# Kernel optimization log

Hardware: AMD Instinct MI355X
Metric: run time of the kernel (lower is better)

## Reference

```python
import jax, jax.numpy as jnp
import numpy as np

B, H, W = 64, 128, 128
K_SIS, K_RANGE = 0.5, 0.3
PSI_SCALE = 0.05
SKIP_W = 0.1
ALPHA_MAX = 0.5
SIGMA, KSIZE = 1.0, 5
DN = ('NCHW', 'OIHW', 'NCHW')


def conv2d(x, w, b, pad):
    y = jax.lax.conv_general_dilated(x, w, (1, 1), [(pad, pad), (pad, pad)], dimension_numbers=DN)
    return y + b[None, :, None, None]


def group_norm(x, groups, gamma, beta, eps=1e-5):
    Bc, C, Hc, Wc = x.shape
    xr = x.reshape(Bc, groups, C // groups, Hc, Wc)
    mu = xr.mean(axis=(2, 3, 4), keepdims=True)
    var = xr.var(axis=(2, 3, 4), keepdims=True)
    xn = ((xr - mu) / jnp.sqrt(var + eps)).reshape(Bc, C, Hc, Wc)
    return xn * gamma[None, :, None, None] + beta[None, :, None, None]


def coords():
    xs = jnp.linspace(-1.0, 1.0, W)
    ys = jnp.linspace(-1.0, 1.0, H)
    X, Y = jnp.meshgrid(xs, ys, indexing='xy')  # (H, W)
    r = jnp.sqrt(X * X + Y * Y)
    phi = jnp.arctan2(Y, X)
    polar = jnp.stack([r, jnp.cos(phi), jnp.sin(phi)], axis=0)  # (3,H,W)
    base_grid = jnp.stack([X, Y], axis=-1)  # (H,W,2)
    return polar, r, base_grid


def gaussian_blur(x):
    off = jnp.arange(KSIZE, dtype=jnp.float32) - (KSIZE - 1) / 2.0
    k1 = jnp.exp(-off * off / (2.0 * SIGMA * SIGMA))
    k1 = k1 / k1.sum()
    p = KSIZE // 2
    xp = jnp.pad(x, ((0, 0), (0, 0), (p, p), (p, p)), mode='reflect')
    xh = jax.lax.conv_general_dilated(xp, k1.reshape(1, 1, 1, KSIZE), (1, 1), [(0, 0), (0, 0)], dimension_numbers=DN)
    return jax.lax.conv_general_dilated(xh, k1.reshape(1, 1, KSIZE, 1), (1, 1), [(0, 0), (0, 0)], dimension_numbers=DN)


def grad_x(a, dx):  # along W (last axis), np.gradient style
    left = a[..., 1:2] - a[..., 0:1]
    mid = (a[..., 2:] - a[..., :-2]) * 0.5
    right = a[..., -1:] - a[..., -2:-1]
    return jnp.concatenate([left, mid, right], axis=-1) / dx


def grad_y(a, dy):  # along H
    top = a[..., 1:2, :] - a[..., 0:1, :]
    mid = (a[..., 2:, :] - a[..., :-2, :]) * 0.5
    bot = a[..., -1:, :] - a[..., -2:-1, :]
    return jnp.concatenate([top, mid, bot], axis=-2) / dy


def soft_clamp(a):
    return ALPHA_MAX * jnp.tanh(a / ALPHA_MAX)


def grid_sample_bilinear_border(img, grid):
    # img (B,1,H,W), grid (B,H,W,2) in [-1,1], align_corners=True, border pad
    Bc, _, Hc, Wc = img.shape
    px = (grid[..., 0] + 1.0) * 0.5 * (Wc - 1)
    py = (grid[..., 1] + 1.0) * 0.5 * (Hc - 1)
    x0 = jnp.floor(px)
    y0 = jnp.floor(py)
    wx = px - x0
    wy = py - y0
    x0i = jnp.clip(x0.astype(jnp.int32), 0, Wc - 1)
    x1i = jnp.clip(x0i + 1, 0, Wc - 1)
    y0i = jnp.clip(y0.astype(jnp.int32), 0, Hc - 1)
    y1i = jnp.clip(y0i + 1, 0, Hc - 1)
    im = img[:, 0]
    bidx = jnp.arange(Bc)[:, None, None]
    g = lambda yy, xx: im[bidx, yy, xx]
    out = (g(y0i, x0i) * (1 - wx) * (1 - wy) + g(y0i, x1i) * wx * (1 - wy)
           + g(y1i, x0i) * (1 - wx) * wy + g(y1i, x1i) * wx * wy)
    return out[:, None, :, :]


def _conv_init(key, shape, scale=None):
    fan_in = shape[1] * shape[2] * shape[3]
    s = scale if scale is not None else 1.0 / np.sqrt(fan_in)
    return jax.random.normal(key, shape, dtype=jnp.float32) * s


def setup_inputs() -> dict:
    key = jax.random.key(0)
    ks = jax.random.split(key, 16)
    d = {'image': jax.random.uniform(ks[0], (B, 1, H, W), dtype=jnp.float32)}
    # KPredictor params
    d['kw1'] = _conv_init(ks[1], (32, 4, 3, 3)); d['kb1'] = jnp.zeros((32,), jnp.float32)
    d['kg1'] = jnp.ones((32,), jnp.float32); d['kbeta1'] = jnp.zeros((32,), jnp.float32)
    d['kw2'] = _conv_init(ks[2], (32, 32, 3, 3)); d['kb2'] = jnp.zeros((32,), jnp.float32)
    d['kg2'] = jnp.ones((32,), jnp.float32); d['kbeta2'] = jnp.zeros((32,), jnp.float32)
    d['kw3'] = _conv_init(ks[3], (16, 32, 3, 3)); d['kb3'] = jnp.zeros((16,), jnp.float32)
    d['kg3'] = jnp.ones((16,), jnp.float32); d['kbeta3'] = jnp.zeros((16,), jnp.float32)
    d['kw4'] = _conv_init(ks[4], (1, 16, 1, 1), scale=0.02); d['kb4'] = jnp.zeros((1,), jnp.float32)
    # PsiResidualPredictor params
    d['pw1'] = _conv_init(ks[5], (16, 4, 3, 3)); d['pb1'] = jnp.zeros((16,), jnp.float32)
    d['pg1'] = jnp.ones((16,), jnp.float32); d['pbeta1'] = jnp.zeros((16,), jnp.float32)
    d['pw2'] = _conv_init(ks[6], (16, 16, 3, 3)); d['pb2'] = jnp.zeros((16,), jnp.float32)
    d['pg2'] = jnp.ones((16,), jnp.float32); d['pbeta2'] = jnp.zeros((16,), jnp.float32)
    d['pw3'] = _conv_init(ks[7], (1, 16, 1, 1), scale=0.02); d['pb3'] = jnp.zeros((1,), jnp.float32)
    return d


def _forward(image, kw1, kb1, kg1, kbeta1, kw2, kb2, kg2, kbeta2, kw3, kb3, kg3, kbeta3,
             kw4, kb4, pw1, pb1, pg1, pbeta1, pw2, pb2, pg2, pbeta2, pw3, pb3):
    polar, theta_abs, base_grid = coords()
    x = jnp.concatenate([image, jnp.broadcast_to(polar[None], (image.shape[0], 3, H, W))], axis=1)
    silu = jax.nn.silu
    # k predictor
    h = silu(group_norm(conv2d(x, kw1, kb1, 1), 8, kg1, kbeta1))
    h = silu(group_norm(conv2d(h, kw2, kb2, 1), 8, kg2, kbeta2))
    h = silu(group_norm(conv2d(h, kw3, kb3, 1), 4, kg3, kbeta3))
    k = K_SIS * (1.0 + K_RANGE * jnp.tanh(conv2d(h, kw4, kb4, 0)))
    # psi residual predictor
    p = silu(group_norm(conv2d(x, pw1, pb1, 1), 4, pg1, pbeta1))
    p = silu(group_norm(conv2d(p, pw2, pb2, 1), 4, pg2, pbeta2))
    psi_res = PSI_SCALE * jnp.tanh(conv2d(p, pw3, pb3, 0))
    psi = k * theta_abs[None, None] + psi_res
    psi_s = gaussian_blur(psi)
    dx = 2.0 / (W - 1)
    dy = 2.0 / (H - 1)
    alpha_x = soft_clamp(grad_x(psi_s, dx))
    alpha_y = soft_clamp(grad_y(psi_s, dy))
    alpha_grid = jnp.stack([alpha_x[:, 0], alpha_y[:, 0]], axis=-1)  # (B,H,W,2)
    beta_grid = jnp.clip(base_grid[None] - alpha_grid, -1.0, 1.0)
    warped = grid_sample_bilinear_border(image, beta_grid)
    source = (1.0 - SKIP_W) * warped + SKIP_W * image
    return source, k, psi, alpha_x, alpha_y


def reference(image, kw1, kb1, kg1, kbeta1, kw2, kb2, kg2, kbeta2, kw3, kb3, kg3, kbeta3,
              kw4, kb4, pw1, pb1, pg1, pbeta1, pw2, pb2, pg2, pbeta2, pw3, pb3):
    return _forward(image, kw1, kb1, kg1, kbeta1, kw2, kb2, kg2, kbeta2, kw3, kb3, kg3,
                    kbeta3, kw4, kb4, pw1, pb1, pg1, pbeta1, pw2, pb2, pg2, pbeta2, pw3, pb3)
```

## Files before the change

kernel.cpp:

```cpp
#include <hip/hip_runtime.h>

static constexpr int H = 128, W = 128, HW = H * W;

typedef __attribute__((ext_vector_type(8))) short short8;
typedef __attribute__((ext_vector_type(4))) float f32x4;
typedef unsigned int uint;
typedef unsigned short ushort;

__device__ __forceinline__ float silu_f(float v) { return v / (1.f + __expf(-v)); }
__device__ __forceinline__ ushort f2bf(float f) {
    uint u = __builtin_bit_cast(uint, f);
    return (ushort)((u + 0x7FFFu + ((u >> 16) & 1u)) >> 16);
}
__device__ __forceinline__ float bf2f(ushort s) {
    return __builtin_bit_cast(float, (uint)s << 16);
}

struct PrepArgs {
    const float *w1, *w2, *w3, *wp1, *wp2;
    float *wt1, *wtp1, *polar, *stats;
    ushort *wpk2h, *wpk2l, *wpk3h, *wpk3l, *wpkph, *wpkpl;
    int nstats;
};

__global__ void prep_k(PrepArgs a) {
    int tid = blockIdx.x * 256 + threadIdx.x;
    int stride = gridDim.x * 256;
    for (int i = tid; i < a.nstats; i += stride) a.stats[i] = 0.f;
    for (int i = tid; i < HW; i += stride) {
        int yy = i >> 7, xx = i & 127;
        float X = -1.f + 2.f * xx / 127.f;
        float Y = -1.f + 2.f * yy / 127.f;
        float r = sqrtf(X * X + Y * Y);
        float inv = (r > 0.f) ? 1.f / r : 0.f;
        a.polar[i] = r;
        a.polar[HW + i] = (r > 0.f) ? X * inv : 1.f;
        a.polar[2 * HW + i] = Y * inv;
    }
    for (int i = tid; i < 4 * 9 * 32; i += stride) {
        int cout = i / 36, rem = i % 36;
        a.wt1[rem * 32 + cout] = a.w1[i];
    }
    for (int i = tid; i < 4 * 9 * 16; i += stride) {
        int cout = i / 36, rem = i % 36;
        a.wtp1[rem * 16 + cout] = a.wp1[i];
    }
    for (int i = tid; i < 9 * 2 * 64 * 8; i += stride) {
        int j = i & 7, l = (i >> 3) & 63, t = i >> 9;
        int q = t >> 1, nt = t & 1;
        int k = (l >> 4) * 8 + j;
        int n = nt * 16 + (l & 15);
        int ky = q / 3, kx = q % 3;
        float w = a.w2[((n * 32 + k) * 3 + ky) * 3 + kx];
        ushort h = f2bf(w);
        a.wpk2h[i] = h;
        a.wpk2l[i] = f2bf(w - bf2f(h));
    }
    for (int i = tid; i < 9 * 64 * 8; i += stride) {
        int j = i & 7, l = (i >> 3) & 63, q = i >> 9;
        int k = (l >> 4) * 8 + j;
        int n = l & 15;
        int ky = q / 3, kx = q % 3;
        float w = a.w3[((n * 32 + k) * 3 + ky) * 3 + kx];
        ushort h = f2bf(w);
        a.wpk3h[i] = h;
        a.wpk3l[i] = f2bf(w - bf2f(h));
    }
    for (int i = tid; i < 9 * 64 * 8; i += stride) {
        int j = i & 7, l = (i >> 3) & 63, q = i >> 9;
        int k = (l >> 4) * 8 + j;
        int cin = k & 15;
        int n = l & 15;
        float w = a.wp2[((n * 16 + cin) * 3 + q / 3) * 3 + q % 3];
        ushort h = f2bf(w);
        a.wpkph[i] = h;
        a.wpkpl[i] = f2bf(w - bf2f(h));
    }
}

template <int COUT, int G>
__global__ __launch_bounds__(256) void conv1_k(
    const float* __restrict__ img, const float* __restrict__ polar,
    const float* __restrict__ wt, const float* __restrict__ bias,
    float* __restrict__ outraw, float* __restrict__ stats) {
    const int tid = threadIdx.x;
    const int y = blockIdx.x * 2 + (tid >> 7);
    const int x = tid & 127;
    const int b = blockIdx.y;

    float acc[COUT];
#pragma unroll
    for (int c = 0; c < COUT; c++) acc[c] = bias[c];

#pragma unroll
    for (int cin = 0; cin < 4; cin++) {
        const float* pl = (cin == 0) ? img + (size_t)b * HW : polar + (size_t)(cin - 1) * HW;
#pragma unroll
        for (int ky = 0; ky < 3; ky++) {
            int yy = y + ky - 1;
            if (yy >= 0 && yy < H) {
                const float* row = pl + yy * W;
                float v1 = row[x];
                float v0 = (x > 0) ? row[x - 1] : 0.f;
                float v2 = (x < 127) ? row[x + 1] : 0.f;
                const float* wr = wt + (cin * 9 + ky * 3) * COUT;
#pragma unroll
                for (int c = 0; c < COUT; c++) {
                    acc[c] = fmaf(wr[c], v0, acc[c]);
                    acc[c] = fmaf(wr[COUT + c], v1, acc[c]);
                    acc[c] = fmaf(wr[2 * COUT + c], v2, acc[c]);
                }
            }
        }
    }

    float4* ob = (float4*)(outraw + ((size_t)b * HW + y * W + x) * COUT);
#pragma unroll
    for (int i = 0; i < COUT / 4; i++)
        ob[i] = make_float4(acc[4 * i], acc[4 * i + 1], acc[4 * i + 2], acc[4 * i + 3]);

    constexpr int CgO = COUT / G;
    __shared__ float sred[4][G][2];
    const int lane = tid & 63, wid = tid >> 6;
#pragma unroll
    for (int g = 0; g < G; g++) {
        float s = 0.f, s2 = 0.f;
#pragma unroll
        for (int c = g * CgO; c < (g + 1) * CgO; c++) { s += acc[c]; s2 += acc[c] * acc[c]; }
#pragma unroll
        for (int off = 32; off > 0; off >>= 1) {
            s += __shfl_down(s, off);
            s2 += __shfl_down(s2, off);
        }
        if (lane == 0) { sred[wid][g][0] = s; sred[wid][g][1] = s2; }
    }
    __syncthreads();
    if (tid < G) {
        float s = 0.f, s2 = 0.f;
#pragma unroll
        for (int w = 0; w < 4; w++) { s += sred[w][tid][0]; s2 += sred[w][tid][1]; }
        atomicAdd(&stats[((size_t)b * G + tid) * 2], s);
        atomicAdd(&stats[((size_t)b * G + tid) * 2 + 1], s2);
    }
}

template <int CIN, int COUT, int Gin, int Gout>
__global__ __launch_bounds__(256, 3) void conv_roll_k(
    const float* __restrict__ raw_in, const float* __restrict__ stats_in,
    const float* __restrict__ gamma, const float* __restrict__ beta,
    const float* __restrict__ bias,
    const short8* __restrict__ wph, const short8* __restrict__ wpl,
    float* __restrict__ outraw, float* __restrict__ stats_out) {

    constexpr int LDSC = 2 * CIN;
    constexpr int SWZM = LDSC / 8 - 1;
    constexpr int NCH8 = CIN / 8;
    constexpr int WN = (COUT == 32) ? 2 : 1;
    constexpr int F = (WN == 2) ? 4 : 2;
    constexpr int ROWS = 8;
    constexpr int ROWB = 128 * LDSC * 2;
    constexpr int CHUNKS = 128 * NCH8 / 256;

    __shared__ __align__(16) ushort ring[3 * 128 * LDSC];
    __shared__ float la[CIN], lc[CIN];

    const int tid = threadIdx.x;
    const int wid = tid >> 6, l = tid & 63;
    const int lm = l & 15, lk = l >> 4;
    const int y0 = blockIdx.x * ROWS;
    const int b = blockIdx.y;
    const int wn = (WN == 2) ? (wid & 1) : 0;
    const int pxb = (WN == 2) ? ((wid >> 1) * 64) : (wid * 32);
    const int ch = wn * 16 + lm;

    if (tid < CIN) {
        constexpr float inv = 1.f / ((CIN / Gin) * (float)HW);
        int g = tid / (CIN / Gin);
        float s = stats_in[((size_t)b * Gin + g) * 2];
        float s2 = stats_in[((size_t)b * Gin + g) * 2 + 1];
        float m = s * inv;
        float rs = rsqrtf(s2 * inv - m * m + 1e-5f);
        float aa = gamma[tid] * rs;
        la[tid] = aa;
        lc[tid] = beta[tid] - m * aa;
    }
    __syncthreads();

    short8 wh[9], wl[9];
#pragma unroll
    for (int q = 0; q < 9; q++) {
        wh[q] = wph[(q * WN + wn) * 64 + l];
        wl[q] = wpl[(q * WN + wn) * 64 + l];
    }
    const float bv = bias[ch];
    const short8 Z8 = {0, 0, 0, 0, 0, 0, 0, 0};
    char* tbw = (char*)ring;

    auto load_row = [&](int ys, float4* g0, float4* g1) {
#pragma unroll
        for (int ck = 0; ck < CHUNKS; ck++) {
            int c = tid + ck * 256;
            int px = c / NCH8, ch8 = c % NCH8;
            const float4* gp = (const float4*)(raw_in + (((size_t)b * HW + ys * W + px) * CIN + ch8 * 8));
            g0[ck] = gp[0];
            g1[ck] = gp[1];
        }
    };
    auto stage_row = [&](int ys, int slot, const float4* g0, const float4* g1) {
#pragma unroll
        for (int ck = 0; ck < CHUNKS; ck++) {
            int c = tid + ck * 256;
            int px = c / NCH8, ch8 = c % NCH8;
            short8 hi8, lo8;
            if (ys >= 0 && ys < H) {
                float vv[8] = {g0[ck].x, g0[ck].y, g0[ck].z, g0[ck].w,
                               g1[ck].x, g1[ck].y, g1[ck].z, g1[ck].w};
#pragma unroll
                for (int e = 0; e < 8; e++) {
                    int cc = ch8 * 8 + e;
                    float f = silu_f(fmaf(vv[e], la[cc], lc[cc]));
                    ushort hb = f2bf(f);
                    hi8[e] = (short)hb;
                    lo8[e] = (short)f2bf(f - bf2f(hb));
                }
            } else {
#pragma unroll
                for (int e = 0; e < 8; e++) { hi8[e] = 0; lo8[e] = 0; }
            }
            int inner = px * LDSC * 2 + ch8 * 16;
            int swz = (px & SWZM) << 4;
            char* sb = tbw + slot * ROWB;
            *(short8*)(sb + (inner ^ swz)) = hi8;
            *(short8*)(sb + ((inner + CIN * 2) ^ swz)) = lo8;
        }
    };

    {
        float4 p0[CHUNKS], p1[CHUNKS];
        for (int pr = 0; pr < 3; pr++) {
            int ys = y0 - 1 + pr;
            if (ys >= 0 && ys < H) load_row(ys, p0, p1);
            stage_row(ys, (ys + 3) % 3, p0, p1);
        }
    }
    __syncthreads();

    float sa = 0.f, sa2 = 0.f;
    float4 g0[CHUNKS], g1[CHUNKS];

    for (int r = 0; r < ROWS; r++) {
        const int y = y0 + r;
        const int ys = y + 2;
        const bool do_stage = (r < ROWS - 1);
        if (do_stage && ys < H) load_row(ys, g0, g1);

        f32x4 acc[F];
#pragma unroll
        for (int f = 0; f < F; f++) acc[f] = (f32x4){0.f, 0.f, 0.f, 0.f};

        const char* sbase[3] = {tbw + ((y + 2) % 3) * ROWB,
                                tbw + ((y + 3) % 3) * ROWB,
                                tbw + ((y + 4) % 3) * ROWB};
#pragma unroll
        for (int q = 0; q < 9; q++) {
            const int ky = q / 3, kx = q % 3;
            const char* sb = sbase[ky];
#pragma unroll
            for (int f = 0; f < F; f++) {
                int xb = pxb + f * 16 + lm + kx - 1;
                bool valid = (xb >= 0) && (xb < 128);
                int xbc = min(max(xb, 0), 127);
                int inner = xbc * LDSC * 2;
                int swz = (xbc & SWZM) << 4;
                if constexpr (CIN == 32) {
                    short8 ah = *(const short8*)(sb + ((inner + lk * 16) ^ swz));
                    short8 al = *(const short8*)(sb + ((inner + (lk + 4) * 16) ^ swz));
                    if (!valid) { ah = Z8; al = Z8; }
                    acc[f] = __builtin_amdgcn_mfma_f32_16x16x32_bf16(ah, wh[q], acc[f], 0, 0, 0);
                    acc[f] = __builtin_amdgcn_mfma_f32_16x16x32_bf16(al, wh[q], acc[f], 0, 0, 0);
                    acc[f] = __builtin_amdgcn_mfma_f32_16x16x32_bf16(ah, wl[q], acc[f], 0, 0, 0);
                } else {
                    short8 a = *(const short8*)(sb + ((inner + lk * 16) ^ swz));
                    if (!valid) a = Z8;
                    acc[f] = __builtin_amdgcn_mfma_f32_16x16x32_bf16(a, wh[q], acc[f], 0, 0, 0);
                    acc[f] = __builtin_amdgcn_mfma_f32_16x16x32_bf16(a, wl[q], acc[f], 0, 0, 0);
                }
            }
        }

#pragma unroll
        for (int f = 0; f < F; f++) {
#pragma unroll
            for (int rr = 0; rr < 4; rr++) {
                int x = pxb + f * 16 + lk * 4 + rr;
                float v = acc[f][rr] + bv;
                outraw[((size_t)b * HW + y * W + x) * COUT + ch] = v;
                sa += v;
                sa2 += v * v;
            }
        }
        __syncthreads();
        if (do_stage) stage_row(ys, (ys + 3) % 3, g0, g1);
        __syncthreads();
    }

    float s = sa, s2 = sa2;
    s += __shfl_xor(s, 16); s2 += __shfl_xor(s2, 16);
    s += __shfl_xor(s, 32); s2 += __shfl_xor(s2, 32);
    constexpr int CgO = COUT / Gout;
#pragma unroll
    for (int m = 1; m < CgO; m <<= 1) { s += __shfl_xor(s, m); s2 += __shfl_xor(s2, m); }
    if (l < 16 && (lm & (CgO - 1)) == 0) {
        int g = ch / CgO;
        atomicAdd(&stats_out[((size_t)b * Gout + g) * 2], s);
        atomicAdd(&stats_out[((size_t)b * Gout + g) * 2 + 1], s2);
    }
}

__global__ void psik_k(const float* __restrict__ h3, const float* __restrict__ p2,
                       const float* __restrict__ kg3, const float* __restrict__ kbeta3,
                       const float* __restrict__ st3,
                       const float* __restrict__ pg2, const float* __restrict__ pbeta2,
                       const float* __restrict__ stp2,
                       const float* __restrict__ kw4, const float* __restrict__ kb4,
                       const float* __restrict__ pw3, const float* __restrict__ pb3,
                       float* __restrict__ outk, float* __restrict__ outpsi, int Bc) {
    int n = blockIdx.x * 256 + threadIdx.x;
    if (n >= Bc * HW) return;
    int b = n >> 14;
    int rem = n & (HW - 1);
    int i = rem >> 7;
    int j = rem & 127;

    constexpr float inv = 1.f / (float)(4 * HW);
    float a3[4], c3[4], ap[4], cp[4];
#pragma unroll
    for (int g = 0; g < 4; g++) {
        float s = st3[((size_t)b * 4 + g) * 2];
        float s2 = st3[((size_t)b * 4 + g) * 2 + 1];
        float m = s * inv;
        a3[g] = rsqrtf(s2 * inv - m * m + 1e-5f);
        c3[g] = m;
        s = stp2[((size_t)b * 4 + g) * 2];
        s2 = stp2[((size_t)b * 4 + g) * 2 + 1];
        m = s * inv;
        ap[g] = rsqrtf(s2 * inv - m * m + 1e-5f);
        cp[g] = m;
    }

    float hv[16], pv[16];
    const float4* hp = (const float4*)(h3 + ((size_t)b * HW + rem) * 16);
    const float4* pp = (const float4*)(p2 + ((size_t)b * HW + rem) * 16);
#pragma unroll
    for (int t = 0; t < 4; t++) {
        float4 u = hp[t];
        hv[4 * t] = u.x; hv[4 * t + 1] = u.y; hv[4 * t + 2] = u.z; hv[4 * t + 3] = u.w;
        float4 w = pp[t];
        pv[4 * t] = w.x; pv[4 * t + 1] = w.y; pv[4 * t + 2] = w.z; pv[4 * t + 3] = w.w;
    }

    float dk = kb4[0], dp = pb3[0];
#pragma unroll
    for (int c = 0; c < 16; c++) {
        int g = c >> 2;
        float a = kg3[c] * a3[g];
        float t = fmaf(hv[c] - c3[g], a, kbeta3[c]);
        dk = fmaf(kw4[c], silu_f(t), dk);
        a = pg2[c] * ap[g];
        t = fmaf(pv[c] - cp[g], a, pbeta2[c]);
        dp = fmaf(pw3[c], silu_f(t), dp);
    }
    float k = 0.5f * (1.f + 0.3f * tanhf(dk));
    float psr = 0.05f * tanhf(dp);
    float X = -1.f + 2.f * j / 127.f;
    float Y = -1.f + 2.f * i / 127.f;
    float r = sqrtf(X * X + Y * Y);
    outk[n] = k;
    outpsi[n] = fmaf(k, r, psr);
}

static __device__ __constant__ float GW0 = 0.40261994689423467f;
static __device__ __constant__ float GW1 = 0.24420134200323348f;
static __device__ __constant__ float GW2 = 0.05448868454964433f;

__global__ void blur_h_k(const float* __restrict__ in, float* __restrict__ out, int B) {
    int n = blockIdx.x * 256 + threadIdx.x;
    if (n >= B * HW) return;
    int j = n & 127;
    const float* row = in + (n - j);
    int jm2 = j - 2; jm2 = jm2 < 0 ? -jm2 : jm2;
    int jm1 = j - 1; jm1 = jm1 < 0 ? -jm1 : jm1;
    int jp1 = j + 1; jp1 = jp1 > 127 ? 254 - jp1 : jp1;
    int jp2 = j + 2; jp2 = jp2 > 127 ? 254 - jp2 : jp2;
    out[n] = GW2 * (row[jm2] + row[jp2]) + GW1 * (row[jm1] + row[jp1]) + GW0 * row[j];
}

__global__ void blur_v_k(const float* __restrict__ in, float* __restrict__ out, int B) {
    int n = blockIdx.x * 256 + threadIdx.x;
    if (n >= B * HW) return;
    int rem = n & (HW - 1);
    int i = rem >> 7;
    int j = rem & 127;
    const float* pl = in + (n - rem) + j;
    int im2 = i - 2; im2 = im2 < 0 ? -im2 : im2;
    int im1 = i - 1; im1 = im1 < 0 ? -im1 : im1;
    int ip1 = i + 1; ip1 = ip1 > 127 ? 254 - ip1 : ip1;
    int ip2 = i + 2; ip2 = ip2 > 127 ? 254 - ip2 : ip2;
    out[n] = GW2 * (pl[im2 * W] + pl[ip2 * W]) + GW1 * (pl[im1 * W] + pl[ip1 * W]) + GW0 * pl[i * W];
}

__global__ void final_k(const float* __restrict__ psis, const float* __restrict__ img,
                        float* __restrict__ osrc, float* __restrict__ oax,
                        float* __restrict__ oay, int B) {
    int n = blockIdx.x * 256 + threadIdx.x;
    if (n >= B * HW) return;
    int rem = n & (HW - 1);
    int i = rem >> 7;
    int j = rem & 127;
    const float* pl = psis + (n - rem);

    float gx;
    if (j == 0)        gx = pl[i * W + 1] - pl[i * W];
    else if (j == 127) gx = pl[i * W + 127] - pl[i * W + 126];
    else               gx = (pl[i * W + j + 1] - pl[i * W + j - 1]) * 0.5f;
    gx *= 63.5f;

    float gy;
    if (i == 0)        gy = pl[W + j] - pl[j];
    else if (i == 127) gy = pl[127 * W + j] - pl[126 * W + j];
    else               gy = (pl[(i + 1) * W + j] - pl[(i - 1) * W + j]) * 0.5f;
    gy *= 63.5f;

    float ax = 0.5f * tanhf(gx * 2.f);
    float ay = 0.5f * tanhf(gy * 2.f);

    float X = -1.f + 2.f * j / 127.f;
    float Y = -1.f + 2.f * i / 127.f;
    float bx = fminf(fmaxf(X - ax, -1.f), 1.f);
    float by = fminf(fmaxf(Y - ay, -1.f), 1.f);
    float px = (bx + 1.f) * 0.5f * 127.f;
    float py = (by + 1.f) * 0.5f * 127.f;
    float x0f = floorf(px), y0f = floorf(py);
    float wx = px - x0f, wy = py - y0f;
    int x0i = min(max((int)x0f, 0), 127);
    int x1i = min(x0i + 1, 127);
    int y0i = min(max((int)y0f, 0), 127);
    int y1i = min(y0i + 1, 127);

    const float* im = img + (size_t)(n >> 14) * HW;
    float v00 = im[y0i * W + x0i], v01 = im[y0i * W + x1i];
    float v10 = im[y1i * W + x0i], v11 = im[y1i * W + x1i];
    float wrp = v00 * (1.f - wx) * (1.f - wy) + v01 * wx * (1.f - wy) +
                v10 * (1.f - wx) * wy + v11 * wx * wy;

    osrc[n] = 0.9f * wrp + 0.1f * im[rem];
    oax[n] = ax;
    oay[n] = ay;
}

extern "C" void kernel_launch(void* const* d_in, const int* in_sizes, int n_in,
                              void* d_out, int out_size, void* d_ws, size_t ws_size,
                              hipStream_t stream) {
    const float* img = (const float*)d_in[0];
    const int B = in_sizes[0] / HW;
    const int npix = B * HW;

    char* base = (char*)d_ws;
    size_t off = 0;
    auto alloc = [&](size_t bytes) {
        char* p = base + off;
        off = (off + bytes + 255) & ~(size_t)255;
        return p;
    };

    float* tmp   = (float*)alloc((size_t)npix * 4);
    float* psis  = (float*)alloc((size_t)npix * 4);
    float* polar = (float*)alloc(3 * HW * 4);
    float* wt1   = (float*)alloc(4 * 9 * 32 * 4);
    float* wtp1  = (float*)alloc(4 * 9 * 16 * 4);
    ushort* wpk2h = (ushort*)alloc(9 * 2 * 64 * 8 * 2);
    ushort* wpk2l = (ushort*)alloc(9 * 2 * 64 * 8 * 2);
    ushort* wpk3h = (ushort*)alloc(9 * 64 * 8 * 2);
    ushort* wpk3l = (ushort*)alloc(9 * 64 * 8 * 2);
    ushort* wpkph = (ushort*)alloc(9 * 64 * 8 * 2);
    ushort* wpkpl = (ushort*)alloc(9 * 64 * 8 * 2);
    int nstats = B * 56;
    float* stats = (float*)alloc((size_t)nstats * 4);
    float* st1  = stats;
    float* st2  = st1 + (size_t)B * 16;
    float* st3  = st2 + (size_t)B * 16;
    float* stp1 = st3 + (size_t)B * 8;
    float* stp2 = stp1 + (size_t)B * 8;
    size_t head = off;

    int BC = B;
    while (BC > 1) {
        size_t need = head + 2 * ((size_t)BC * HW * 32 * 4 + 256);
        if (need <= ws_size) break;
        BC >>= 1;
    }
    float* R  = (float*)alloc((size_t)BC * HW * 32 * 4);
    float* R2 = (float*)alloc((size_t)BC * HW * 32 * 4);
    float* h3R = R;
    float* p2R = R + (size_t)BC * HW * 16;
    float* RpR = R2;

    float* outsrc = (float*)d_out;
    float* outk   = outsrc + (size_t)npix;
    float* outpsi = outk + (size_t)npix;
    float* outax  = outpsi + (size_t)npix;
    float* outay  = outax + (size_t)npix;

    PrepArgs pa;
    pa.w1 = (const float*)d_in[1]; pa.w2 = (const float*)d_in[5];
    pa.w3 = (const float*)d_in[9]; pa.wp1 = (const float*)d_in[15];
    pa.wp2 = (const float*)d_in[19];
    pa.wt1 = wt1; pa.wtp1 = wtp1; pa.polar = polar; pa.stats = stats;
    pa.wpk2h = wpk2h; pa.wpk2l = wpk2l; pa.wpk3h = wpk3h; pa.wpk3l = wpk3l;
    pa.wpkph = wpkph; pa.wpkpl = wpkpl; pa.nstats = nstats;
    prep_k<<<128, 256, 0, stream>>>(pa);

    for (int b0 = 0; b0 < B; b0 += BC) {
        const float* imgc = img + (size_t)b0 * HW;
        dim3 cg1(H / 2, BC), cgr(H / 8, BC);

        conv1_k<32, 8><<<cg1, 256, 0, stream>>>(imgc, polar, wt1, (const float*)d_in[2],
                                                R, st1 + (size_t)b0 * 16);
        conv_roll_k<32, 32, 8, 8><<<cgr, 256, 0, stream>>>(
            R, st1 + (size_t)b0 * 16, (const float*)d_in[3], (const float*)d_in[4],
            (const float*)d_in[6], (const short8*)wpk2h, (const short8*)wpk2l,
            R2, st2 + (size_t)b0 * 16);
        conv_roll_k<32, 16, 8, 4><<<cgr, 256, 0, stream>>>(
            R2, st2 + (size_t)b0 * 16, (const float*)d_in[7], (const float*)d_in[8],
            (const float*)d_in[10], (const short8*)wpk3h, (const short8*)wpk3l,
            h3R, st3 + (size_t)b0 * 8);

        conv1_k<16, 4><<<cg1, 256, 0, stream>>>(imgc, polar, wtp1, (const float*)d_in[16],
                                                RpR, stp1 + (size_t)b0 * 8);
        conv_roll_k<16, 16, 4, 4><<<cgr, 256, 0, stream>>>(
            RpR, stp1 + (size_t)b0 * 8, (const float*)d_in[17], (const float*)d_in[18],
            (const float*)d_in[20], (const short8*)wpkph, (const short8*)wpkpl,
            p2R, stp2 + (size_t)b0 * 8);

        int pgrid = (BC * HW + 255) / 256;
        psik_k<<<pgrid, 256, 0, stream>>>(h3R, p2R,
            (const float*)d_in[11], (const float*)d_in[12], st3 + (size_t)b0 * 8,
            (const float*)d_in[21], (const float*)d_in[22], stp2 + (size_t)b0 * 8,
            (const float*)d_in[13], (const float*)d_in[14],
            (const float*)d_in[23], (const float*)d_in[24],
            outk + (size_t)b0 * HW, outpsi + (size_t)b0 * HW, BC);
    }

    int pgrid = (npix + 255) / 256;
    blur_h_k<<<pgrid, 256, 0, stream>>>(outpsi, tmp, B);
    blur_v_k<<<pgrid, 256, 0, stream>>>(tmp, psis, B);
    final_k<<<pgrid, 256, 0, stream>>>(psis, img, outsrc, outax, outay, B);
}
```

Measured before the change: 438.4 us.

## Fuse psi head, blur, gradient and warp into one tiled tail kernel

Replaces the psi/k kernel and the separate horizontal blur, vertical blur and final warp kernels with a single tail kernel. Each block computes a 32-row band of psi plus a 3-row reflected halo in shared memory, then blurs and differentiates it on chip, removing the intermediate global round-trips. It also doubles the rows per block in the rolling 3x3 conv, replaces round-to-nearest bf16 hi/lo splitting with truncation, and raises wave priority around the MFMA loop. The cost is recomputing the halo rows and running fewer, larger tail blocks (4 per batch image).

```diff
diff --git a/kernel.cpp b/kernel.cpp
--- a/kernel.cpp
+++ b/kernel.cpp
@@ -157,7 +157,7 @@
     constexpr int NCH8 = CIN / 8;
     constexpr int WN = (COUT == 32) ? 2 : 1;
     constexpr int F = (WN == 2) ? 4 : 2;
-    constexpr int ROWS = 8;
+    constexpr int ROWS = 16;
     constexpr int ROWB = 128 * LDSC * 2;
     constexpr int CHUNKS = 128 * NCH8 / 256;
 
@@ -219,9 +219,11 @@
                 for (int e = 0; e < 8; e++) {
                     int cc = ch8 * 8 + e;
                     float f = silu_f(fmaf(vv[e], la[cc], lc[cc]));
-                    ushort hb = f2bf(f);
-                    hi8[e] = (short)hb;
-                    lo8[e] = (short)f2bf(f - bf2f(hb));
+                    uint u = __builtin_bit_cast(uint, f);
+                    uint uh = u & 0xFFFF0000u;
+                    float r = f - __builtin_bit_cast(float, uh);
+                    hi8[e] = (short)(u >> 16);
+                    lo8[e] = (short)(__builtin_bit_cast(uint, r) >> 16);
                 }
             } else {
 #pragma unroll
@@ -261,6 +263,7 @@
         const char* sbase[3] = {tbw + ((y + 2) % 3) * ROWB,
                                 tbw + ((y + 3) % 3) * ROWB,
                                 tbw + ((y + 4) % 3) * ROWB};
+        __builtin_amdgcn_s_setprio(1);
 #pragma unroll
         for (int q = 0; q < 9; q++) {
             const int ky = q / 3, kx = q % 3;
@@ -287,6 +290,7 @@
                 }
             }
         }
+        __builtin_amdgcn_s_setprio(0);
 
 #pragma unroll
         for (int f = 0; f < F; f++) {
@@ -317,20 +321,28 @@
     }
 }
 
-__global__ void psik_k(const float* __restrict__ h3, const float* __restrict__ p2,
-                       const float* __restrict__ kg3, const float* __restrict__ kbeta3,
-                       const float* __restrict__ st3,
-                       const float* __restrict__ pg2, const float* __restrict__ pbeta2,
-                       const float* __restrict__ stp2,
-                       const float* __restrict__ kw4, const float* __restrict__ kb4,
-                       const float* __restrict__ pw3, const float* __restrict__ pb3,
-                       float* __restrict__ outk, float* __restrict__ outpsi, int Bc) {
-    int n = blockIdx.x * 256 + threadIdx.x;
-    if (n >= Bc * HW) return;
-    int b = n >> 14;
-    int rem = n & (HW - 1);
-    int i = rem >> 7;
-    int j = rem & 127;
+static __device__ __constant__ float GW0 = 0.40261994689423467f;
+static __device__ __constant__ float GW1 = 0.24420134200323348f;
+static __device__ __constant__ float GW2 = 0.05448868454964433f;
+
+__global__ __launch_bounds__(512) void tail_k(
+    const float* __restrict__ h3, const float* __restrict__ p2,
+    const float* __restrict__ img,
+    const float* __restrict__ kg3, const float* __restrict__ kbeta3,
+    const float* __restrict__ st3,
+    const float* __restrict__ pg2, const float* __restrict__ pbeta2,
+    const float* __restrict__ stp2,
+    const float* __restrict__ kw4, const float* __restrict__ kb4,
+    const float* __restrict__ pw3, const float* __restrict__ pb3,
+    float* __restrict__ osrc, float* __restrict__ outk,
+    float* __restrict__ outpsi, float* __restrict__ oax,
+    float* __restrict__ oay) {
+    __shared__ float psiA[38 * 128];
+    __shared__ float psiB[38 * 128];
+
+    const int tid = threadIdx.x;
+    const int y0 = blockIdx.x * 32;
+    const int b = blockIdx.y;
 
     constexpr float inv = 1.f / (float)(4 * HW);
     float a3[4], c3[4], ap[4], cp[4];
@@ -348,114 +360,111 @@
         cp[g] = m;
     }
 
-    float hv[16], pv[16];
-    const float4* hp = (const float4*)(h3 + ((size_t)b * HW + rem) * 16);
-    const float4* pp = (const float4*)(p2 + ((size_t)b * HW + rem) * 16);
-#pragma unroll
-    for (int t = 0; t < 4; t++) {
-        float4 u = hp[t];
-        hv[4 * t] = u.x; hv[4 * t + 1] = u.y; hv[4 * t + 2] = u.z; hv[4 * t + 3] = u.w;
-        float4 w = pp[t];
-        pv[4 * t] = w.x; pv[4 * t + 1] = w.y; pv[4 * t + 2] = w.z; pv[4 * t + 3] = w.w;
-    }
-
-    float dk = kb4[0], dp = pb3[0];
-#pragma unroll
-    for (int c = 0; c < 16; c++) {
-        int g = c >> 2;
-        float a = kg3[c] * a3[g];
-        float t = fmaf(hv[c] - c3[g], a, kbeta3[c]);
-        dk = fmaf(kw4[c], silu_f(t), dk);
-        a = pg2[c] * ap[g];
-        t = fmaf(pv[c] - cp[g], a, pbeta2[c]);
-        dp = fmaf(pw3[c], silu_f(t), dp);
-    }
-    float k = 0.5f * (1.f + 0.3f * tanhf(dk));
-    float psr = 0.05f * tanhf(dp);
-    float X = -1.f + 2.f * j / 127.f;
-    float Y = -1.f + 2.f * i / 127.f;
-    float r = sqrtf(X * X + Y * Y);
-    outk[n] = k;
-    outpsi[n] = fmaf(k, r, psr);
-}
-
-static __device__ __constant__ float GW0 = 0.40261994689423467f;
-static __device__ __constant__ float GW1 = 0.24420134200323348f;
-static __device__ __constant__ float GW2 = 0.05448868454964433f;
-
-__global__ void blur_h_k(const float* __restrict__ in, float* __restrict__ out, int B) {
-    int n = blockIdx.x * 256 + threadIdx.x;
-    if (n >= B * HW) return;
-    int j = n & 127;
-    const float* row = in + (n - j);
-    int jm2 = j - 2; jm2 = jm2 < 0 ? -jm2 : jm2;
-    int jm1 = j - 1; jm1 = jm1 < 0 ? -jm1 : jm1;
-    int jp1 = j + 1; jp1 = jp1 > 127 ? 254 - jp1 : jp1;
-    int jp2 = j + 2; jp2 = jp2 > 127 ? 254 - jp2 : jp2;
-    out[n] = GW2 * (row[jm2] + row[jp2]) + GW1 * (row[jm1] + row[jp1]) + GW0 * row[j];
-}
-
-__global__ void blur_v_k(const float* __restrict__ in, float* __restrict__ out, int B) {
-    int n = blockIdx.x * 256 + threadIdx.x;
-    if (n >= B * HW) return;
-    int rem = n & (HW - 1);
-    int i = rem >> 7;
-    int j = rem & 127;
-    const float* pl = in + (n - rem) + j;
-    int im2 = i - 2; im2 = im2 < 0 ? -im2 : im2;
-    int im1 = i - 1; im1 = im1 < 0 ? -im1 : im1;
-    int ip1 = i + 1; ip1 = ip1 > 127 ? 254 - ip1 : ip1;
-    int ip2 = i + 2; ip2 = ip2 > 127 ? 254 - ip2 : ip2;
-    out[n] = GW2 * (pl[im2 * W] + pl[ip2 * W]) + GW1 * (pl[im1 * W] + pl[ip1 * W]) + GW0 * pl[i * W];
-}
-
-__global__ void final_k(const float* __restrict__ psis, const float* __restrict__ img,
-                        float* __restrict__ osrc, float* __restrict__ oax,
-                        float* __restrict__ oay, int B) {
-    int n = blockIdx.x * 256 + threadIdx.x;
-    if (n >= B * HW) return;
-    int rem = n & (HW - 1);
-    int i = rem >> 7;
-    int j = rem & 127;
-    const float* pl = psis + (n - rem);
-
-    float gx;
-    if (j == 0)        gx = pl[i * W + 1] - pl[i * W];
-    else if (j == 127) gx = pl[i * W + 127] - pl[i * W + 126];
-    else               gx = (pl[i * W + j + 1] - pl[i * W + j - 1]) * 0.5f;
-    gx *= 63.5f;
-
-    float gy;
-    if (i == 0)        gy = pl[W + j] - pl[j];
-    else if (i == 127) gy = pl[127 * W + j] - pl[126 * W + j];
-    else               gy = (pl[(i + 1) * W + j] - pl[(i - 1) * W + j]) * 0.5f;
-    gy *= 63.5f;
-
-    float ax = 0.5f * tanhf(gx * 2.f);
-    float ay = 0.5f * tanhf(gy * 2.f);
-
-    float X = -1.f + 2.f * j / 127.f;
-    float Y = -1.f + 2.f * i / 127.f;
-    float bx = fminf(fmaxf(X - ax, -1.f), 1.f);
-    float by = fminf(fmaxf(Y - ay, -1.f), 1.f);
-    float px = (bx + 1.f) * 0.5f * 127.f;
-    float py = (by + 1.f) * 0.5f * 127.f;
-    float x0f = floorf(px), y0f = floorf(py);
-    float wx = px - x0f, wy = py - y0f;
-    int x0i = min(max((int)x0f, 0), 127);
-    int x1i = min(x0i + 1, 127);
-    int y0i = min(max((int)y0f, 0), 127);
-    int y1i = min(y0i + 1, 127);
-
-    const float* im = img + (size_t)(n >> 14) * HW;
-    float v00 = im[y0i * W + x0i], v01 = im[y0i * W + x1i];
-    float v10 = im[y1i * W + x0i], v11 = im[y1i * W + x1i];
-    float wrp = v00 * (1.f - wx) * (1.f - wy) + v01 * wx * (1.f - wy) +
-                v10 * (1.f - wx) * wy + v11 * wx * wy;
-
-    osrc[n] = 0.9f * wrp + 0.1f * im[rem];
-    oax[n] = ax;
-    oay[n] = ay;
+    for (int idx = tid; idx < 38 * 128; idx += 512) {
+        int s = idx >> 7, j = idx & 127;
+        int g = y0 - 3 + s;
+        g = (g < 0) ? -g : (g > 127 ? 254 - g : g);
+        int rem = g * W + j;
+
+        float hv[16], pv[16];
+        const float4* hp = (const float4*)(h3 + ((size_t)b * HW + rem) * 16);
+        const float4* pp = (const float4*)(p2 + ((size_t)b * HW + rem) * 16);
+#pragma unroll
+        for (int t = 0; t < 4; t++) {
+            float4 u = hp[t];
+            hv[4 * t] = u.x; hv[4 * t + 1] = u.y; hv[4 * t + 2] = u.z; hv[4 * t + 3] = u.w;
+            float4 w = pp[t];
+            pv[4 * t] = w.x; pv[4 * t + 1] = w.y; pv[4 * t + 2] = w.z; pv[4 * t + 3] = w.w;
+        }
+        float dk = kb4[0], dp = pb3[0];
+#pragma unroll
+        for (int c = 0; c < 16; c++) {
+            int gg = c >> 2;
+            float a = kg3[c] * a3[gg];
+            float t = fmaf(hv[c] - c3[gg], a, kbeta3[c]);
+            dk = fmaf(kw4[c], silu_f(t), dk);
+            a = pg2[c] * ap[gg];
+            t = fmaf(pv[c] - cp[gg], a, pbeta2[c]);
+            dp = fmaf(pw3[c], silu_f(t), dp);
+        }
+        float k = 0.5f * (1.f + 0.3f * tanhf(dk));
+        float psr = 0.05f * tanhf(dp);
+        float X = -1.f + 2.f * j / 127.f;
+        float Y = -1.f + 2.f * g / 127.f;
+        float r = sqrtf(X * X + Y * Y);
+        float psi = fmaf(k, r, psr);
+        psiA[idx] = psi;
+        if (s >= 3 && s <= 34) {
+            int n = (size_t)b * HW + rem;
+            outk[n] = k;
+            outpsi[n] = psi;
+        }
+    }
+    __syncthreads();
+
+    for (int idx = tid; idx < 38 * 128; idx += 512) {
+        int s = idx >> 7, j = idx & 127;
+        const float* row = psiA + s * 128;
+        int jm2 = j - 2; jm2 = jm2 < 0 ? -jm2 : jm2;
+        int jm1 = j - 1; jm1 = jm1 < 0 ? -jm1 : jm1;
+        int jp1 = j + 1; jp1 = jp1 > 127 ? 254 - jp1 : jp1;
+        int jp2 = j + 2; jp2 = jp2 > 127 ? 254 - jp2 : jp2;
+        psiB[idx] = GW2 * (row[jm2] + row[jp2]) + GW1 * (row[jm1] + row[jp1]) + GW0 * row[j];
+    }
+    __syncthreads();
+
+    for (int idx = tid; idx < 34 * 128; idx += 512) {
+        int s = (idx >> 7) + 2, j = idx & 127;
+        psiA[s * 128 + j] = GW2 * (psiB[(s - 2) * 128 + j] + psiB[(s + 2) * 128 + j]) +
+                            GW1 * (psiB[(s - 1) * 128 + j] + psiB[(s + 1) * 128 + j]) +
+                            GW0 * psiB[s * 128 + j];
+    }
+    __syncthreads();
+
+    const float* im = img + (size_t)b * HW;
+    for (int idx = tid; idx < 32 * 128; idx += 512) {
+        int r = idx >> 7, j = idx & 127;
+        int y = y0 + r, s = r + 3;
+        const float* ps = psiA + s * 128;
+
+        float gx;
+        if (j == 0)        gx = ps[1] - ps[0];
+        else if (j == 127) gx = ps[127] - ps[126];
+        else               gx = (ps[j + 1] - ps[j - 1]) * 0.5f;
+        gx *= 63.5f;
+
+        float gy;
+        if (y == 0)        gy = psiA[(s + 1) * 128 + j] - ps[j];
+        else if (y == 127) gy = ps[j] - psiA[(s - 1) * 128 + j];
+        else               gy = (psiA[(s + 1) * 128 + j] - psiA[(s - 1) * 128 + j]) * 0.5f;
+        gy *= 63.5f;
+
+        float ax = 0.5f * tanhf(gx * 2.f);
+        float ay = 0.5f * tanhf(gy * 2.f);
+
+        float X = -1.f + 2.f * j / 127.f;
+        float Y = -1.f + 2.f * y / 127.f;
+        float bx = fminf(fmaxf(X - ax, -1.f), 1.f);
+        float by = fminf(fmaxf(Y - ay, -1.f), 1.f);
+        float px = (bx + 1.f) * 0.5f * 127.f;
+        float py = (by + 1.f) * 0.5f * 127.f;
+        float x0f = floorf(px), y0f = floorf(py);
+        float wx = px - x0f, wy = py - y0f;
+        int x0i = min(max((int)x0f, 0), 127);
+        int x1i = min(x0i + 1, 127);
+        int y0i = min(max((int)y0f, 0), 127);
+        int y1i = min(y0i + 1, 127);
+
+        float v00 = im[y0i * W + x0i], v01 = im[y0i * W + x1i];
+        float v10 = im[y1i * W + x0i], v11 = im[y1i * W + x1i];
+        float wrp = v00 * (1.f - wx) * (1.f - wy) + v01 * wx * (1.f - wy) +
+                    v10 * (1.f - wx) * wy + v11 * wx * wy;
+
+        int n = (size_t)b * HW + y * W + j;
+        osrc[n] = 0.9f * wrp + 0.1f * im[y * W + j];
+        oax[n] = ax;
+        oay[n] = ay;
+    }
 }
 
 extern "C" void kernel_launch(void* const* d_in, const int* in_sizes, int n_in,
@@ -473,8 +482,6 @@
         return p;
     };
 
-    float* tmp   = (float*)alloc((size_t)npix * 4);
-    float* psis  = (float*)alloc((size_t)npix * 4);
     float* polar = (float*)alloc(3 * HW * 4);
     float* wt1   = (float*)alloc(4 * 9 * 32 * 4);
     float* wtp1  = (float*)alloc(4 * 9 * 16 * 4);
@@ -522,7 +529,7 @@
 
     for (int b0 = 0; b0 < B; b0 += BC) {
         const float* imgc = img + (size_t)b0 * HW;
-        dim3 cg1(H / 2, BC), cgr(H / 8, BC);
+        dim3 cg1(H / 2, BC), cgr(H / 16, BC);
 
         conv1_k<32, 8><<<cg1, 256, 0, stream>>>(imgc, polar, wt1, (const float*)d_in[2],
                                                 R, st1 + (size_t)b0 * 16);
@@ -542,17 +549,14 @@
             (const float*)d_in[20], (const short8*)wpkph, (const short8*)wpkpl,
             p2R, stp2 + (size_t)b0 * 8);
 
-        int pgrid = (BC * HW + 255) / 256;
-        psik_k<<<pgrid, 256, 0, stream>>>(h3R, p2R,
+        tail_k<<<dim3(4, BC), 512, 0, stream>>>(
+            h3R, p2R, imgc,
             (const float*)d_in[11], (const float*)d_in[12], st3 + (size_t)b0 * 8,
             (const float*)d_in[21], (const float*)d_in[22], stp2 + (size_t)b0 * 8,
             (const float*)d_in[13], (const float*)d_in[14],
             (const float*)d_in[23], (const float*)d_in[24],
-            outk + (size_t)b0 * HW, outpsi + (size_t)b0 * HW, BC);
-    }
-
-    int pgrid = (npix + 255) / 256;
-    blur_h_k<<<pgrid, 256, 0, stream>>>(outpsi, tmp, B);
-    blur_v_k<<<pgrid, 256, 0, stream>>>(tmp, psis, B);
-    final_k<<<pgrid, 256, 0, stream>>>(psis, img, outsrc, outax, outay, B);
-}
+            outsrc + (size_t)b0 * HW, outk + (size_t)b0 * HW,
+            outpsi + (size_t)b0 * HW, outax + (size_t)b0 * HW,
+            outay + (size_t)b0 * HW);
+    }
+}
```

Result: slower. 502.9 us (+14.7%).
